# Kernel optimization log

Hardware: AMD Instinct MI355X
Metric: run time of the kernel (lower is better)

## Reference

```python
import jax, jax.numpy as jnp
import numpy as np


def setup_inputs() -> dict:
    key = jax.random.key(0)
    k1, k2 = jax.random.split(key)
    decoder_output = jax.random.normal(k1, (8, 2048, 128), dtype=jnp.float32)
    encoder_output = jax.random.normal(k2, (8, 4096, 128), dtype=jnp.float32)
    return {"decoder_output": decoder_output, "encoder_output": encoder_output}


def reference(decoder_output, encoder_output):
    # Unscaled Luong (general dot) attention.
    # scores: [B, Tq, Tk] = dec [B,Tq,D] . enc [B,Tk,D]^T
    scores = jnp.einsum('bqd,bkd->bqk', decoder_output, encoder_output)
    attention = jax.nn.softmax(scores, axis=-1)
    # context: [B, Tq, D] = attn [B,Tq,Tk] . enc [B,Tk,D]
    context = jnp.einsum('bqk,bkd->bqd', attention, encoder_output)
    return (context, attention)
```

## Files before the change

kernel.cpp:

```cpp
#include <hip/hip_runtime.h>

using f16   = _Float16;
using f16x4 = __attribute__((ext_vector_type(4))) _Float16;
using f16x8 = __attribute__((ext_vector_type(8))) _Float16;
using f32x4 = __attribute__((ext_vector_type(4))) float;

#define NBATCH 8
#define TQ 2048
#define TK 4096
#define DD 128
#define QBLK 32
#define KBLK 128
#define NT (TK / KBLK)
#define CTX_ELEMS ((size_t)NBATCH * TQ * DD)
#define PWLD 56
#define CTLD 132
#define KTB 36864

__device__ __forceinline__ int koff(int t, int d) {
    const int blk = ((t >> 2) & 3) ^ ((d >> 4) & 3);
    return (t >> 4) * 2304 + (d >> 4) * 288 + blk * 72 + (t & 3) * 16 + (d & 15);
}

__device__ __forceinline__ f16x4 ds_read_tr16(unsigned addr) {
    f16x4 d;
    asm volatile("ds_read_b64_tr_b16 %0, %1" : "=v"(d) : "v"(addr));
    return d;
}

__device__ __forceinline__ void pipe_barrier() {
    asm volatile("s_waitcnt lgkmcnt(0)" ::: "memory");
    __builtin_amdgcn_s_barrier();
    __builtin_amdgcn_sched_barrier(0);
}

__global__ __launch_bounds__(256)
void cvt_kernel(const float* __restrict__ in, f16* __restrict__ out) {
    const size_t i = ((size_t)blockIdx.x * 256 + threadIdx.x) * 8;
    const float4 a = *(const float4*)(in + i);
    const float4 b = *(const float4*)(in + i + 4);
    f16x8 h;
    h[0] = (f16)a.x; h[1] = (f16)a.y; h[2] = (f16)a.z; h[3] = (f16)a.w;
    h[4] = (f16)b.x; h[5] = (f16)b.y; h[6] = (f16)b.z; h[7] = (f16)b.w;
    *(f16x8*)(out + i) = h;
}

template<bool F16SRC>
__global__ __launch_bounds__(512, 4)
void luong_attn_kernel(const float* __restrict__ dec,
                       const void* __restrict__ encv,
                       float* __restrict__ out) {
    __shared__ __align__(16) char LDSbuf[2 * KTB + 1024];
    f16*   Kt0   = (f16*)LDSbuf;
    f16*   Kt1   = (f16*)(LDSbuf + KTB);
    f16*   PwAll = (f16*)(LDSbuf + KTB);
    float* Zbuf  = (float*)(LDSbuf + 2 * KTB);

    const int tid  = threadIdx.x;
    const int wid  = tid >> 6;
    const int lane = tid & 63;
    const int lo   = lane & 15;
    const int g    = lane >> 4;
    const int qg   = wid & 1;
    const int th   = wid >> 1;

    const int b     = blockIdx.x & 7;
    const int qbase = (blockIdx.x >> 3) * QBLK;

    const float* encB32 = F16SRC ? nullptr : ((const float*)encv) + (size_t)b * TK * DD;
    const f16*   encB16 = F16SRC ? ((const f16*)encv) + (size_t)b * TK * DD : nullptr;
    float* attn = out + CTX_ELEMS + ((size_t)b * TQ + qbase) * TK;

    f16x8  s16[4];
    float4 s32[8];
    auto loadR = [&](int tile) {
        if constexpr (F16SRC) {
            const f16* src = encB16 + (size_t)tile * KBLK * DD;
            #pragma unroll
            for (int i = 0; i < 4; ++i) {
                const int c = tid + (i << 9);
                s16[i] = *(const f16x8*)(src + (c >> 4) * DD + ((c & 15) << 3));
            }
        } else {
            const float* src = encB32 + (size_t)tile * KBLK * DD;
            #pragma unroll
            for (int i = 0; i < 8; ++i) {
                const int c = tid + (i << 9);
                s32[i] = *(const float4*)(src + (c >> 5) * DD + ((c & 31) << 2));
            }
        }
    };
    auto writeR = [&](f16* Kt) {
        if constexpr (F16SRC) {
            #pragma unroll
            for (int i = 0; i < 4; ++i) {
                const int c = tid + (i << 9);
                *(f16x8*)&Kt[koff(c >> 4, (c & 15) << 3)] = s16[i];
            }
        } else {
            #pragma unroll
            for (int i = 0; i < 8; ++i) {
                const int c = tid + (i << 9);
                f16x4 h;
                h[0] = (f16)s32[i].x; h[1] = (f16)s32[i].y;
                h[2] = (f16)s32[i].z; h[3] = (f16)s32[i].w;
                *(f16x4*)&Kt[koff(c >> 5, (c & 31) << 2)] = h;
            }
        }
    };

    f16x8 qfh[2][4];
    #pragma unroll
    for (int h2 = 0; h2 < 2; ++h2) {
        const float* qp = dec + ((size_t)b * TQ + qbase + h2 * 16 + lo) * DD;
        #pragma unroll
        for (int kk = 0; kk < 4; ++kk) {
            const float4 x = *(const float4*)(qp + kk * 32 + g * 8);
            const float4 y = *(const float4*)(qp + kk * 32 + g * 8 + 4);
            f16x8 h;
            h[0] = (f16)x.x; h[1] = (f16)x.y; h[2] = (f16)x.z; h[3] = (f16)x.w;
            h[4] = (f16)y.x; h[5] = (f16)y.y; h[6] = (f16)y.z; h[7] = (f16)y.w;
            qfh[h2][kk] = h;
        }
    }

    float Zp0[4] = {0.f, 0.f, 0.f, 0.f};
    float Zp1[4] = {0.f, 0.f, 0.f, 0.f};

    loadR(0);
    writeR(Kt0);
    pipe_barrier();
    #pragma unroll 1
    for (int tile = 0; tile < NT; ++tile) {
        f16* Ktc = (tile & 1) ? Kt1 : Kt0;
        f16* Ktn = (tile & 1) ? Kt0 : Kt1;
        if (tile + 1 < NT) loadR(tile + 1);

        f32x4 S0 = {0.f, 0.f, 0.f, 0.f};
        f32x4 S1 = {0.f, 0.f, 0.f, 0.f};
        const int t = wid * 16 + lo;
        __builtin_amdgcn_s_setprio(1);
        #pragma unroll
        for (int kk = 0; kk < 4; ++kk) {
            const f16x8 bf = *(const f16x8*)&Ktc[koff(t, kk * 32 + g * 8)];
            S0 = __builtin_amdgcn_mfma_f32_16x16x32_f16(qfh[0][kk], bf, S0, 0, 0, 0);
            S1 = __builtin_amdgcn_mfma_f32_16x16x32_f16(qfh[1][kk], bf, S1, 0, 0, 0);
        }
        __builtin_amdgcn_s_setprio(0);

        if (tile + 1 < NT) writeR(Ktn);
        #pragma unroll
        for (int r = 0; r < 4; ++r) {
            Zp0[r] += __expf(S0[r]);
            Zp1[r] += __expf(S1[r]);
        }
        pipe_barrier();
    }

    #pragma unroll
    for (int r = 0; r < 4; ++r) {
        Zp0[r] += __shfl_xor(Zp0[r], 1); Zp1[r] += __shfl_xor(Zp1[r], 1);
        Zp0[r] += __shfl_xor(Zp0[r], 2); Zp1[r] += __shfl_xor(Zp1[r], 2);
        Zp0[r] += __shfl_xor(Zp0[r], 4); Zp1[r] += __shfl_xor(Zp1[r], 4);
        Zp0[r] += __shfl_xor(Zp0[r], 8); Zp1[r] += __shfl_xor(Zp1[r], 8);
    }
    if (lo == 0) {
        #pragma unroll
        for (int r = 0; r < 4; ++r) {
            Zbuf[wid * 32 + 4 * g + r]      = Zp0[r];
            Zbuf[wid * 32 + 16 + 4 * g + r] = Zp1[r];
        }
    }
    __syncthreads();
    float iz[4];
    #pragma unroll
    for (int r = 0; r < 4; ++r) {
        float z = 0.f;
        #pragma unroll
        for (int w = 0; w < 8; ++w) z += Zbuf[w * 32 + qg * 16 + 4 * g + r];
        iz[r] = 1.0f / z;
    }
    __syncthreads();

    f16x8 qf2[4];
    if (qg == 0) {
        #pragma unroll
        for (int kk = 0; kk < 4; ++kk) qf2[kk] = qfh[0][kk];
    } else {
        #pragma unroll
        for (int kk = 0; kk < 4; ++kk) qf2[kk] = qfh[1][kk];
    }

    f32x4 ctx[8];
    #pragma unroll
    for (int n = 0; n < 8; ++n) { f32x4 z = {0.f, 0.f, 0.f, 0.f}; ctx[n] = z; }

    f16* Pw = PwAll + wid * 16 * PWLD;
    const unsigned KtBase = (unsigned)(size_t)&Kt0[0];
    const int t0 = th * 32 + g * 8;

    #pragma unroll 1
    for (int tile = 0; tile < NT; ++tile) {
        loadR(tile);
        writeR(Kt0);
        pipe_barrier();

        f32x4 S[2];
        #pragma unroll
        for (int f = 0; f < 2; ++f) { f32x4 z = {0.f, 0.f, 0.f, 0.f}; S[f] = z; }
        __builtin_amdgcn_s_setprio(1);
        #pragma unroll
        for (int f = 0; f < 2; ++f) {
            const int t = th * 32 + f * 16 + lo;
            #pragma unroll
            for (int kk = 0; kk < 4; ++kk) {
                const f16x8 bf = *(const f16x8*)&Kt0[koff(t, kk * 32 + g * 8)];
                S[f] = __builtin_amdgcn_mfma_f32_16x16x32_f16(qf2[kk], bf, S[f], 0, 0, 0);
            }
        }
        __builtin_amdgcn_s_setprio(0);

        #pragma unroll
        for (int f = 0; f < 2; ++f) {
            const int tloc = f * 16 + lo;
            #pragma unroll
            for (int r = 0; r < 4; ++r)
                Pw[(4 * g + r) * PWLD + tloc] = (f16)(__expf(S[f][r]) * iz[r]);
        }
        asm volatile("" ::: "memory");

        {
            const int qq  = lane >> 2;
            const int grp = lane & 3;
            const f16x8 pr = *(const f16x8*)&Pw[qq * PWLD + grp * 8];
            f32x4 a0, a1;
            a0[0] = (float)pr[0]; a0[1] = (float)pr[1]; a0[2] = (float)pr[2]; a0[3] = (float)pr[3];
            a1[0] = (float)pr[4]; a1[1] = (float)pr[5]; a1[2] = (float)pr[6]; a1[3] = (float)pr[7];
            float* dst = attn + (size_t)(qg * 16 + qq) * TK + tile * KBLK + th * 32 + grp * 8;
            __builtin_nontemporal_store(a0, (f32x4*)dst);
            __builtin_nontemporal_store(a1, (f32x4*)(dst + 4));
        }

        const f16x8 pa = *(const f16x8*)&Pw[lo * PWLD + g * 8];
        __builtin_amdgcn_s_setprio(1);
        #pragma unroll
        for (int nh = 0; nh < 2; ++nh) {
            f16x4 tr0[4], tr1[4];
            #pragma unroll
            for (int n4 = 0; n4 < 4; ++n4) {
                const int n = nh * 4 + n4;
                const int blk0 = ((t0 >> 2) & 3) ^ (n & 3);
                const int blk1 = (((t0 + 4) >> 2) & 3) ^ (n & 3);
                const unsigned a0 =
                    KtBase + (unsigned)(((t0 >> 4) * 2304 + n * 288 + blk0 * 72) * 2) + lo * 8;
                const unsigned a1 =
                    KtBase + (unsigned)(((t0 >> 4) * 2304 + n * 288 + blk1 * 72) * 2) + lo * 8;
                tr0[n4] = ds_read_tr16(a0);
                tr1[n4] = ds_read_tr16(a1);
            }
            asm volatile("s_waitcnt lgkmcnt(0)" ::: "memory");
            __builtin_amdgcn_sched_barrier(0);
            #pragma unroll
            for (int n4 = 0; n4 < 4; ++n4) {
                f16x8 vb;
                vb[0] = tr0[n4][0]; vb[1] = tr0[n4][1]; vb[2] = tr0[n4][2]; vb[3] = tr0[n4][3];
                vb[4] = tr1[n4][0]; vb[5] = tr1[n4][1]; vb[6] = tr1[n4][2]; vb[7] = tr1[n4][3];
                ctx[nh * 4 + n4] =
                    __builtin_amdgcn_mfma_f32_16x16x32_f16(pa, vb, ctx[nh * 4 + n4], 0, 0, 0);
            }
        }
        __builtin_amdgcn_s_setprio(0);
        pipe_barrier();
    }

    float* CT = (float*)LDSbuf;
    const int q32 = qg * 16 + 4 * g;
    if (th >= 2) {
        #pragma unroll
        for (int n = 0; n < 8; ++n)
            #pragma unroll
            for (int r = 0; r < 4; ++r)
                CT[((th - 2) * 32 + q32 + r) * CTLD + n * 16 + lo] = ctx[n][r];
    }
    __syncthreads();
    if (th < 2) {
        #pragma unroll
        for (int n = 0; n < 8; ++n)
            #pragma unroll
            for (int r = 0; r < 4; ++r)
                ctx[n][r] += CT[(th * 32 + q32 + r) * CTLD + n * 16 + lo];
    }
    __syncthreads();
    if (th == 1) {
        #pragma unroll
        for (int n = 0; n < 8; ++n)
            #pragma unroll
            for (int r = 0; r < 4; ++r)
                CT[(q32 + r) * CTLD + n * 16 + lo] = ctx[n][r];
    }
    __syncthreads();
    if (th == 0) {
        #pragma unroll
        for (int n = 0; n < 8; ++n)
            #pragma unroll
            for (int r = 0; r < 4; ++r)
                out[((size_t)b * TQ + qbase + q32 + r) * DD + n * 16 + lo] =
                    ctx[n][r] + CT[(q32 + r) * CTLD + n * 16 + lo];
    }
}

extern "C" void kernel_launch(void* const* d_in, const int* in_sizes, int n_in,
                              void* d_out, int out_size, void* d_ws, size_t ws_size,
                              hipStream_t stream) {
    (void)in_sizes; (void)n_in; (void)out_size;
    const float* dec = (const float*)d_in[0];
    const float* enc = (const float*)d_in[1];
    float* out = (float*)d_out;
    dim3 grid(NBATCH * (TQ / QBLK));
    dim3 block(512);

    const size_t encN = (size_t)NBATCH * TK * DD;
    if (ws_size >= encN * sizeof(f16)) {
        f16* encH = (f16*)d_ws;
        hipLaunchKernelGGL(cvt_kernel, dim3((unsigned)(encN / (256 * 8))), dim3(256),
                           0, stream, enc, encH);
        hipLaunchKernelGGL((luong_attn_kernel<true>), grid, block, 0, stream,
                           dec, (const void*)encH, out);
    } else {
        hipLaunchKernelGGL((luong_attn_kernel<false>), grid, block, 0, stream,
                           dec, (const void*)enc, out);
    }
}
```

Baseline: 122.8 us.

## Double query block to 64 with 1024-thread blocks and double-buffer second pass

Raises the query tile from 32 to 64 rows per block, using 16 waves, so each encoder tile loaded into LDS is reused by twice as many queries. This halves the redundant encoder reads across blocks. The second (PV) pass now double-buffers the K tile: it prefetches the next tile during compute and moves P staging to a dedicated LDS region. The cost is larger LDS per block and 1024-thread blocks, which limits occupancy, plus a reload of the query fragments from global memory.

```diff
diff --git a/kernel.cpp b/kernel.cpp
--- a/kernel.cpp
+++ b/kernel.cpp
@@ -9,13 +9,14 @@
 #define TQ 2048
 #define TK 4096
 #define DD 128
-#define QBLK 32
+#define QBLK 64
 #define KBLK 128
 #define NT (TK / KBLK)
 #define CTX_ELEMS ((size_t)NBATCH * TQ * DD)
 #define PWLD 56
 #define CTLD 132
 #define KTB 36864
+#define PWB (16 * 16 * PWLD * 2)
 
 __device__ __forceinline__ int koff(int t, int d) {
     const int blk = ((t >> 2) & 3) ^ ((d >> 4) & 3);
@@ -46,23 +47,23 @@
 }
 
 template<bool F16SRC>
-__global__ __launch_bounds__(512, 4)
+__global__ __launch_bounds__(1024, 4)
 void luong_attn_kernel(const float* __restrict__ dec,
                        const void* __restrict__ encv,
                        float* __restrict__ out) {
-    __shared__ __align__(16) char LDSbuf[2 * KTB + 1024];
-    f16*   Kt0   = (f16*)LDSbuf;
-    f16*   Kt1   = (f16*)(LDSbuf + KTB);
-    f16*   PwAll = (f16*)(LDSbuf + KTB);
-    float* Zbuf  = (float*)(LDSbuf + 2 * KTB);
+    __shared__ __align__(16) char LDSbuf[2 * KTB + PWB + 2048];
+    f16*   PwAll = (f16*)(LDSbuf + 2 * KTB);
+    float* Zbuf  = (float*)(LDSbuf + 2 * KTB + PWB);
 
     const int tid  = threadIdx.x;
     const int wid  = tid >> 6;
     const int lane = tid & 63;
     const int lo   = lane & 15;
     const int g    = lane >> 4;
-    const int qg   = wid & 1;
-    const int th   = wid >> 1;
+    const int tcol  = wid & 7;
+    const int qpair = wid >> 3;
+    const int qg4 = wid & 3;
+    const int th4 = wid >> 2;
 
     const int b     = blockIdx.x & 7;
     const int qbase = (blockIdx.x >> 3) * QBLK;
@@ -71,21 +72,21 @@
     const f16*   encB16 = F16SRC ? ((const f16*)encv) + (size_t)b * TK * DD : nullptr;
     float* attn = out + CTX_ELEMS + ((size_t)b * TQ + qbase) * TK;
 
-    f16x8  s16[4];
-    float4 s32[8];
+    f16x8  s16[2];
+    float4 s32[4];
     auto loadR = [&](int tile) {
         if constexpr (F16SRC) {
             const f16* src = encB16 + (size_t)tile * KBLK * DD;
             #pragma unroll
-            for (int i = 0; i < 4; ++i) {
-                const int c = tid + (i << 9);
+            for (int i = 0; i < 2; ++i) {
+                const int c = tid + (i << 10);
                 s16[i] = *(const f16x8*)(src + (c >> 4) * DD + ((c & 15) << 3));
             }
         } else {
             const float* src = encB32 + (size_t)tile * KBLK * DD;
             #pragma unroll
-            for (int i = 0; i < 8; ++i) {
-                const int c = tid + (i << 9);
+            for (int i = 0; i < 4; ++i) {
+                const int c = tid + (i << 10);
                 s32[i] = *(const float4*)(src + (c >> 5) * DD + ((c & 31) << 2));
             }
         }
@@ -93,14 +94,14 @@
     auto writeR = [&](f16* Kt) {
         if constexpr (F16SRC) {
             #pragma unroll
+            for (int i = 0; i < 2; ++i) {
+                const int c = tid + (i << 10);
+                *(f16x8*)&Kt[koff(c >> 4, (c & 15) << 3)] = s16[i];
+            }
+        } else {
+            #pragma unroll
             for (int i = 0; i < 4; ++i) {
-                const int c = tid + (i << 9);
-                *(f16x8*)&Kt[koff(c >> 4, (c & 15) << 3)] = s16[i];
-            }
-        } else {
-            #pragma unroll
-            for (int i = 0; i < 8; ++i) {
-                const int c = tid + (i << 9);
+                const int c = tid + (i << 10);
                 f16x4 h;
                 h[0] = (f16)s32[i].x; h[1] = (f16)s32[i].y;
                 h[2] = (f16)s32[i].z; h[3] = (f16)s32[i].w;
@@ -108,11 +109,13 @@
             }
         }
     };
+    f16* Kt0 = (f16*)LDSbuf;
+    f16* Kt1 = (f16*)(LDSbuf + KTB);
 
     f16x8 qfh[2][4];
     #pragma unroll
     for (int h2 = 0; h2 < 2; ++h2) {
-        const float* qp = dec + ((size_t)b * TQ + qbase + h2 * 16 + lo) * DD;
+        const float* qp = dec + ((size_t)b * TQ + qbase + qpair * 32 + h2 * 16 + lo) * DD;
         #pragma unroll
         for (int kk = 0; kk < 4; ++kk) {
             const float4 x = *(const float4*)(qp + kk * 32 + g * 8);
@@ -138,7 +141,7 @@
 
         f32x4 S0 = {0.f, 0.f, 0.f, 0.f};
         f32x4 S1 = {0.f, 0.f, 0.f, 0.f};
-        const int t = wid * 16 + lo;
+        const int t = tcol * 16 + lo;
         __builtin_amdgcn_s_setprio(1);
         #pragma unroll
         for (int kk = 0; kk < 4; ++kk) {
@@ -172,23 +175,32 @@
         }
     }
     __syncthreads();
+
+    f16x8 qf2[4];
+    {
+        const float* qp2 = dec + ((size_t)b * TQ + qbase + qg4 * 16 + lo) * DD;
+        #pragma unroll
+        for (int kk = 0; kk < 4; ++kk) {
+            const float4 x = *(const float4*)(qp2 + kk * 32 + g * 8);
+            const float4 y = *(const float4*)(qp2 + kk * 32 + g * 8 + 4);
+            f16x8 h;
+            h[0] = (f16)x.x; h[1] = (f16)x.y; h[2] = (f16)x.z; h[3] = (f16)x.w;
+            h[4] = (f16)y.x; h[5] = (f16)y.y; h[6] = (f16)y.z; h[7] = (f16)y.w;
+            qf2[kk] = h;
+        }
+    }
     float iz[4];
-    #pragma unroll
-    for (int r = 0; r < 4; ++r) {
-        float z = 0.f;
-        #pragma unroll
-        for (int w = 0; w < 8; ++w) z += Zbuf[w * 32 + qg * 16 + 4 * g + r];
-        iz[r] = 1.0f / z;
-    }
-    __syncthreads();
-
-    f16x8 qf2[4];
-    if (qg == 0) {
-        #pragma unroll
-        for (int kk = 0; kk < 4; ++kk) qf2[kk] = qfh[0][kk];
-    } else {
-        #pragma unroll
-        for (int kk = 0; kk < 4; ++kk) qf2[kk] = qfh[1][kk];
+    {
+        const int qpair2 = qg4 >> 1;
+        const int qloc   = (qg4 & 1) * 16 + 4 * g;
+        #pragma unroll
+        for (int r = 0; r < 4; ++r) {
+            float z = 0.f;
+            #pragma unroll
+            for (int t8 = 0; t8 < 8; ++t8)
+                z += Zbuf[(qpair2 * 8 + t8) * 32 + qloc + r];
+            iz[r] = 1.0f / z;
+        }
     }
 
     f32x4 ctx[8];
@@ -196,14 +208,18 @@
     for (int n = 0; n < 8; ++n) { f32x4 z = {0.f, 0.f, 0.f, 0.f}; ctx[n] = z; }
 
     f16* Pw = PwAll + wid * 16 * PWLD;
-    const unsigned KtBase = (unsigned)(size_t)&Kt0[0];
-    const int t0 = th * 32 + g * 8;
-
+    const unsigned KtLow = (unsigned)(size_t)&LDSbuf[0];
+    const int t0 = th4 * 32 + g * 8;
+
+    loadR(0);
+    writeR(Kt0);
+    pipe_barrier();
+    int cur = 0;
     #pragma unroll 1
     for (int tile = 0; tile < NT; ++tile) {
-        loadR(tile);
-        writeR(Kt0);
-        pipe_barrier();
+        if (tile + 1 < NT) loadR(tile + 1);
+        const f16* Ktc = (const f16*)(LDSbuf + cur * KTB);
+        const unsigned kbase = KtLow + (unsigned)(cur * KTB);
 
         f32x4 S[2];
         #pragma unroll
@@ -211,10 +227,10 @@
         __builtin_amdgcn_s_setprio(1);
         #pragma unroll
         for (int f = 0; f < 2; ++f) {
-            const int t = th * 32 + f * 16 + lo;
+            const int t = th4 * 32 + f * 16 + lo;
             #pragma unroll
             for (int kk = 0; kk < 4; ++kk) {
-                const f16x8 bf = *(const f16x8*)&Kt0[koff(t, kk * 32 + g * 8)];
+                const f16x8 bf = *(const f16x8*)&Ktc[koff(t, kk * 32 + g * 8)];
                 S[f] = __builtin_amdgcn_mfma_f32_16x16x32_f16(qf2[kk], bf, S[f], 0, 0, 0);
             }
         }
@@ -236,7 +252,7 @@
             f32x4 a0, a1;
             a0[0] = (float)pr[0]; a0[1] = (float)pr[1]; a0[2] = (float)pr[2]; a0[3] = (float)pr[3];
             a1[0] = (float)pr[4]; a1[1] = (float)pr[5]; a1[2] = (float)pr[6]; a1[3] = (float)pr[7];
-            float* dst = attn + (size_t)(qg * 16 + qq) * TK + tile * KBLK + th * 32 + grp * 8;
+            float* dst = attn + (size_t)(qg4 * 16 + qq) * TK + tile * KBLK + th4 * 32 + grp * 8;
             __builtin_nontemporal_store(a0, (f32x4*)dst);
             __builtin_nontemporal_store(a1, (f32x4*)(dst + 4));
         }
@@ -252,9 +268,9 @@
                 const int blk0 = ((t0 >> 2) & 3) ^ (n & 3);
                 const int blk1 = (((t0 + 4) >> 2) & 3) ^ (n & 3);
                 const unsigned a0 =
-                    KtBase + (unsigned)(((t0 >> 4) * 2304 + n * 288 + blk0 * 72) * 2) + lo * 8;
+                    kbase + (unsigned)(((t0 >> 4) * 2304 + n * 288 + blk0 * 72) * 2) + lo * 8;
                 const unsigned a1 =
-                    KtBase + (unsigned)(((t0 >> 4) * 2304 + n * 288 + blk1 * 72) * 2) + lo * 8;
+                    kbase + (unsigned)(((t0 >> 4) * 2304 + n * 288 + blk1 * 72) * 2) + lo * 8;
                 tr0[n4] = ds_read_tr16(a0);
                 tr1[n4] = ds_read_tr16(a1);
             }
@@ -270,42 +286,46 @@
             }
         }
         __builtin_amdgcn_s_setprio(0);
+
+        if (tile + 1 < NT)
+            writeR((f16*)(LDSbuf + ((cur ^ 1) * KTB)));
         pipe_barrier();
+        cur ^= 1;
     }
 
     float* CT = (float*)LDSbuf;
-    const int q32 = qg * 16 + 4 * g;
-    if (th >= 2) {
+    const int q64 = qg4 * 16 + 4 * g;
+    if (th4 >= 2) {
         #pragma unroll
         for (int n = 0; n < 8; ++n)
             #pragma unroll
             for (int r = 0; r < 4; ++r)
-                CT[((th - 2) * 32 + q32 + r) * CTLD + n * 16 + lo] = ctx[n][r];
+                CT[((th4 - 2) * 64 + q64 + r) * CTLD + n * 16 + lo] = ctx[n][r];
     }
     __syncthreads();
-    if (th < 2) {
+    if (th4 < 2) {
         #pragma unroll
         for (int n = 0; n < 8; ++n)
             #pragma unroll
             for (int r = 0; r < 4; ++r)
-                ctx[n][r] += CT[(th * 32 + q32 + r) * CTLD + n * 16 + lo];
+                ctx[n][r] += CT[(th4 * 64 + q64 + r) * CTLD + n * 16 + lo];
     }
     __syncthreads();
-    if (th == 1) {
+    if (th4 == 1) {
         #pragma unroll
         for (int n = 0; n < 8; ++n)
             #pragma unroll
             for (int r = 0; r < 4; ++r)
-                CT[(q32 + r) * CTLD + n * 16 + lo] = ctx[n][r];
+                CT[(q64 + r) * CTLD + n * 16 + lo] = ctx[n][r];
     }
     __syncthreads();
-    if (th == 0) {
+    if (th4 == 0) {
         #pragma unroll
         for (int n = 0; n < 8; ++n)
             #pragma unroll
             for (int r = 0; r < 4; ++r)
-                out[((size_t)b * TQ + qbase + q32 + r) * DD + n * 16 + lo] =
-                    ctx[n][r] + CT[(q32 + r) * CTLD + n * 16 + lo];
+                out[((size_t)b * TQ + qbase + q64 + r) * DD + n * 16 + lo] =
+                    ctx[n][r] + CT[(q64 + r) * CTLD + n * 16 + lo];
     }
 }
 
@@ -317,7 +337,7 @@
     const float* enc = (const float*)d_in[1];
     float* out = (float*)d_out;
     dim3 grid(NBATCH * (TQ / QBLK));
-    dim3 block(512);
+    dim3 block(1024);
 
     const size_t encN = (size_t)NBATCH * TK * DD;
     if (ws_size >= encN * sizeof(f16)) {
```

Measured after the change: 178.3 us. +45.1%, slower.

## Load K fragments directly from global into registers in f16 score pass

Applied to the files above, without the earlier changes.

In the f16-source path, the first pass that computes softmax normalizers now loads each wave's K fragments straight from global memory into registers. It double-buffers them across two tiles using explicit vmcnt waits, replacing the LDS staging and the per-tile block barriers. This is meant to remove the LDS write/read traffic and the synchronisation from the normalizer loop. In exchange it uses more VGPRs, and K tiles may be fetched redundantly across waves and blocks, relying on the caches.

```diff
diff --git a/kernel.cpp b/kernel.cpp
--- a/kernel.cpp
+++ b/kernel.cpp
@@ -28,11 +28,19 @@
     return d;
 }
 
+__device__ __forceinline__ f16x8 gload8h(const f16* p) {
+    f16x8 r;
+    asm volatile("global_load_dwordx4 %0, %1, off" : "=v"(r) : "v"(p) : "memory");
+    return r;
+}
+
 __device__ __forceinline__ void pipe_barrier() {
     asm volatile("s_waitcnt lgkmcnt(0)" ::: "memory");
     __builtin_amdgcn_s_barrier();
     __builtin_amdgcn_sched_barrier(0);
 }
+#define VMWAIT(N) do { asm volatile("s_waitcnt vmcnt(" #N ")" ::: "memory"); \
+                       __builtin_amdgcn_sched_barrier(0); } while (0)
 
 __global__ __launch_bounds__(256)
 void cvt_kernel(const float* __restrict__ in, f16* __restrict__ out) {
@@ -127,34 +135,89 @@
     float Zp0[4] = {0.f, 0.f, 0.f, 0.f};
     float Zp1[4] = {0.f, 0.f, 0.f, 0.f};
 
-    loadR(0);
-    writeR(Kt0);
-    pipe_barrier();
-    #pragma unroll 1
-    for (int tile = 0; tile < NT; ++tile) {
-        f16* Ktc = (tile & 1) ? Kt1 : Kt0;
-        f16* Ktn = (tile & 1) ? Kt0 : Kt1;
-        if (tile + 1 < NT) loadR(tile + 1);
-
-        f32x4 S0 = {0.f, 0.f, 0.f, 0.f};
-        f32x4 S1 = {0.f, 0.f, 0.f, 0.f};
-        const int t = wid * 16 + lo;
-        __builtin_amdgcn_s_setprio(1);
-        #pragma unroll
-        for (int kk = 0; kk < 4; ++kk) {
-            const f16x8 bf = *(const f16x8*)&Ktc[koff(t, kk * 32 + g * 8)];
-            S0 = __builtin_amdgcn_mfma_f32_16x16x32_f16(qfh[0][kk], bf, S0, 0, 0, 0);
-            S1 = __builtin_amdgcn_mfma_f32_16x16x32_f16(qfh[1][kk], bf, S1, 0, 0, 0);
-        }
-        __builtin_amdgcn_s_setprio(0);
-
-        if (tile + 1 < NT) writeR(Ktn);
-        #pragma unroll
-        for (int r = 0; r < 4; ++r) {
-            Zp0[r] += __expf(S0[r]);
-            Zp1[r] += __expf(S1[r]);
-        }
+    if constexpr (F16SRC) {
+        const f16* kp = encB16 + (size_t)(wid * 16 + lo) * DD;
+        f16x8 curf[4], nxtf[4];
+        #pragma unroll
+        for (int kk = 0; kk < 4; ++kk)
+            curf[kk] = gload8h(kp + kk * 32 + g * 8);
+
+        #pragma unroll 1
+        for (int tile = 0; tile < NT; tile += 2) {
+            #pragma unroll
+            for (int kk = 0; kk < 4; ++kk)
+                nxtf[kk] = gload8h(kp + (size_t)(tile + 1) * KBLK * DD + kk * 32 + g * 8);
+            VMWAIT(4);
+
+            f32x4 S0 = {0.f, 0.f, 0.f, 0.f};
+            f32x4 S1 = {0.f, 0.f, 0.f, 0.f};
+            __builtin_amdgcn_s_setprio(1);
+            #pragma unroll
+            for (int kk = 0; kk < 4; ++kk) {
+                S0 = __builtin_amdgcn_mfma_f32_16x16x32_f16(qfh[0][kk], curf[kk], S0, 0, 0, 0);
+                S1 = __builtin_amdgcn_mfma_f32_16x16x32_f16(qfh[1][kk], curf[kk], S1, 0, 0, 0);
+            }
+            __builtin_amdgcn_s_setprio(0);
+            #pragma unroll
+            for (int r = 0; r < 4; ++r) {
+                Zp0[r] += __expf(S0[r]);
+                Zp1[r] += __expf(S1[r]);
+            }
+
+            if (tile + 2 < NT) {
+                #pragma unroll
+                for (int kk = 0; kk < 4; ++kk)
+                    curf[kk] = gload8h(kp + (size_t)(tile + 2) * KBLK * DD + kk * 32 + g * 8);
+                VMWAIT(4);
+            } else {
+                VMWAIT(0);
+            }
+
+            f32x4 T0 = {0.f, 0.f, 0.f, 0.f};
+            f32x4 T1 = {0.f, 0.f, 0.f, 0.f};
+            __builtin_amdgcn_s_setprio(1);
+            #pragma unroll
+            for (int kk = 0; kk < 4; ++kk) {
+                T0 = __builtin_amdgcn_mfma_f32_16x16x32_f16(qfh[0][kk], nxtf[kk], T0, 0, 0, 0);
+                T1 = __builtin_amdgcn_mfma_f32_16x16x32_f16(qfh[1][kk], nxtf[kk], T1, 0, 0, 0);
+            }
+            __builtin_amdgcn_s_setprio(0);
+            #pragma unroll
+            for (int r = 0; r < 4; ++r) {
+                Zp0[r] += __expf(T0[r]);
+                Zp1[r] += __expf(T1[r]);
+            }
+        }
+    } else {
+        loadR(0);
+        writeR(Kt0);
         pipe_barrier();
+        #pragma unroll 1
+        for (int tile = 0; tile < NT; ++tile) {
+            f16* Ktc = (tile & 1) ? Kt1 : Kt0;
+            f16* Ktn = (tile & 1) ? Kt0 : Kt1;
+            if (tile + 1 < NT) loadR(tile + 1);
+
+            f32x4 S0 = {0.f, 0.f, 0.f, 0.f};
+            f32x4 S1 = {0.f, 0.f, 0.f, 0.f};
+            const int t = wid * 16 + lo;
+            __builtin_amdgcn_s_setprio(1);
+            #pragma unroll
+            for (int kk = 0; kk < 4; ++kk) {
+                const f16x8 bf = *(const f16x8*)&Ktc[koff(t, kk * 32 + g * 8)];
+                S0 = __builtin_amdgcn_mfma_f32_16x16x32_f16(qfh[0][kk], bf, S0, 0, 0, 0);
+                S1 = __builtin_amdgcn_mfma_f32_16x16x32_f16(qfh[1][kk], bf, S1, 0, 0, 0);
+            }
+            __builtin_amdgcn_s_setprio(0);
+
+            if (tile + 1 < NT) writeR(Ktn);
+            #pragma unroll
+            for (int r = 0; r < 4; ++r) {
+                Zp0[r] += __expf(S0[r]);
+                Zp1[r] += __expf(S1[r]);
+            }
+            pipe_barrier();
+        }
     }
 
     #pragma unroll
```

After: 141.9 us. 15.5% more time.
